# Kernel tuning notes

Measured on AMD Instinct MI355X. Metric: run time of the kernel, lower is better.

## Reference

```python
import jax, jax.numpy as jnp
import numpy as np

N_RAYS = 131072
N_SAMPLES = 64
N_IMPORTANCE = 128
NEAR, FAR = 2.0, 6.0


def setup_inputs() -> dict:
    key = jax.random.key(0)
    k1, k2, k3, k4 = jax.random.split(key, 4)
    rays_o = jax.random.normal(k1, (N_RAYS, 3), dtype=jnp.float32)
    rays_d = jax.random.normal(k2, (N_RAYS, 3), dtype=jnp.float32)
    # z_vals must be increasing along the sample axis (coarse sample output)
    z_vals = NEAR + (FAR - NEAR) * jnp.sort(
        jax.random.uniform(k3, (N_RAYS, N_SAMPLES), dtype=jnp.float32), axis=-1)
    weights = jax.random.uniform(k4, (N_RAYS, N_SAMPLES), dtype=jnp.float32)
    return {"rays_o": rays_o, "rays_d": rays_d, "z_vals": z_vals, "weights": weights}


def fine_sample(rays_o, rays_d, z_vals, weights):
    # z_vals: [N, S], weights: [N, S]; det=True (perturb == 0.0)
    z_mid = 0.5 * (z_vals[..., 1:] + z_vals[..., :-1])          # [N, S-1]
    w = weights[..., 1:-1] + 1e-5                               # [N, S-2]
    pdf = w / jnp.sum(w, axis=-1, keepdims=True)
    cdf = jnp.cumsum(pdf, axis=-1)
    cdf = jnp.concatenate([jnp.zeros_like(cdf[..., :1]), cdf], axis=-1)  # [N, S-1]

    u = jnp.linspace(0.0, 1.0, N_IMPORTANCE, dtype=cdf.dtype)
    u = jnp.broadcast_to(u, (cdf.shape[0], N_IMPORTANCE))       # [N, Ni]

    # per-ray binary search (right side), matching torch.searchsorted(right=True)
    inds = jax.vmap(lambda c, uu: jnp.searchsorted(c, uu, side='right'))(cdf, u)
    below = jnp.maximum(inds - 1, 0)
    above = jnp.minimum(inds, cdf.shape[-1] - 1)

    cdf_b = jnp.take_along_axis(cdf, below, axis=-1)
    cdf_a = jnp.take_along_axis(cdf, above, axis=-1)
    bins_b = jnp.take_along_axis(z_mid, below, axis=-1)
    bins_a = jnp.take_along_axis(z_mid, above, axis=-1)

    denom = cdf_a - cdf_b
    denom = jnp.where(denom < 1e-5, jnp.ones_like(denom), denom)
    t = (u - cdf_b) / denom
    z_samples = bins_b + t * (bins_a - bins_b)                  # [N, Ni]

    z_all = jnp.sort(jnp.concatenate([z_vals, z_samples], axis=-1), axis=-1)  # [N, S+Ni]
    pts = rays_o[:, None, :] + rays_d[:, None, :] * z_all[..., None]          # [N, S+Ni, 3]
    return pts, z_all


def reference(rays_o, rays_d, z_vals, weights):
    return fine_sample(rays_o, rays_d, z_vals, weights)
```

## Files before the change

### kernel.cpp

```cpp
#include <hip/hip_runtime.h>
#include <hip/hip_bf16.h>

#define S   64
#define NI  128
#define NT  192
#define WPB 4

__global__ __launch_bounds__(256) void nerf_fine_sample(
    const float* __restrict__ rays_o,
    const float* __restrict__ rays_d,
    const float* __restrict__ z_vals,
    const float* __restrict__ weights,
    float* __restrict__ out_pts,
    float* __restrict__ out_z)
{
    const int lane = threadIdx.x & 63;
    const int w    = threadIdx.x >> 6;
    const int ray  = blockIdx.x * WPB + w;

    __shared__ float s_zvals[WPB][S];
    __shared__ float s_zmid [WPB][S];
    __shared__ float s_cdf  [WPB][S];
    __shared__ float s_zs   [WPB][NI];
    __shared__ float s_zall [WPB][NT];
    __shared__ float s_od   [WPB][8];

    const float zv = z_vals[(size_t)ray * S + lane];
    const float wt = weights[(size_t)ray * S + lane];
    s_zvals[w][lane] = zv;
    if (lane < 6) {
        s_od[w][lane] = (lane < 3) ? rays_o[(size_t)ray * 3 + lane]
                                   : rays_d[(size_t)ray * 3 + (lane - 3)];
    }

    float zvn = __shfl_down(zv, 1);
    if (lane < S - 1) s_zmid[w][lane] = 0.5f * (zv + zvn);

    float x = (lane >= 1 && lane <= S - 2) ? (wt + 1e-5f) : 0.0f;
    float v = x;
    #pragma unroll
    for (int off = 1; off < 64; off <<= 1) {
        float n = __shfl_up(v, off);
        if (lane >= off) v += n;
    }
    const float total = __shfl(v, 63);
    const float inv   = 1.0f / total;
    if (lane <= S - 2) s_cdf[w][lane] = v * inv;

    __syncthreads();

    {
        const float* cdf  = s_cdf[w];
        const float* zmid = s_zmid[w];
        const float step = 1.0f / 127.0f;
        #pragma unroll
        for (int r = 0; r < 2; ++r) {
            const int k = lane + r * 64;
            float u = (k == NI - 1) ? 1.0f : (float)k * step;
            int lo = 0, hi = S - 1;
            while (lo < hi) {
                int m = (lo + hi) >> 1;
                if (cdf[m] <= u) lo = m + 1; else hi = m;
            }
            const int below = (lo > 0) ? lo - 1 : 0;
            const int above = (lo < S - 2) ? lo : S - 2;
            const float cb = cdf[below], ca = cdf[above];
            const float bb = zmid[below], ba = zmid[above];
            float denom = ca - cb;
            if (denom < 1e-5f) denom = 1.0f;
            const float t = (u - cb) / denom;
            s_zs[w][k] = bb + t * (ba - bb);
        }
    }
    __syncthreads();

    {
        const float* zs = s_zs[w];
        int lo = 0, hi = NI;
        while (lo < hi) {
            int m = (lo + hi) >> 1;
            if (zs[m] < zv) lo = m + 1; else hi = m;
        }
        s_zall[w][lane + lo] = zv;
    }
    {
        const float* za = s_zvals[w];
        #pragma unroll
        for (int r = 0; r < 2; ++r) {
            const int j = lane + r * 64;
            const float z = s_zs[w][j];
            int lo = 0, hi = S;
            while (lo < hi) {
                int m = (lo + hi) >> 1;
                if (za[m] <= z) lo = m + 1; else hi = m;
            }
            s_zall[w][j + lo] = z;
        }
    }
    __syncthreads();

    const float ox = s_od[w][0], oy = s_od[w][1], oz = s_od[w][2];
    const float dx = s_od[w][3], dy = s_od[w][4], dz = s_od[w][5];

    if (lane < NT / 4) {
        float4 q = ((const float4*)s_zall[w])[lane];
        ((float4*)(out_z + (size_t)ray * NT))[lane] = q;
    }

    float* po = out_pts + (size_t)ray * NT * 3;
    #pragma unroll
    for (int r = 0; r < 3; ++r) {
        const int e4 = lane + r * 64;
        if (e4 < 144) {
            float4 q;
            float qv[4];
            #pragma unroll
            for (int c = 0; c < 4; ++c) {
                const int e = e4 * 4 + c;
                const int s = e / 3;
                const int comp = e - 3 * s;
                const float z = s_zall[w][s];
                const float o = (comp == 0) ? ox : ((comp == 1) ? oy : oz);
                const float d = (comp == 0) ? dx : ((comp == 1) ? dy : dz);
                qv[c] = o + d * z;
            }
            q.x = qv[0]; q.y = qv[1]; q.z = qv[2]; q.w = qv[3];
            ((float4*)po)[e4] = q;
        }
    }
}

extern "C" void kernel_launch(void* const* d_in, const int* in_sizes, int n_in,
                              void* d_out, int out_size, void* d_ws, size_t ws_size,
                              hipStream_t stream) {
    const float* rays_o  = (const float*)d_in[0];
    const float* rays_d  = (const float*)d_in[1];
    const float* z_vals  = (const float*)d_in[2];
    const float* weights = (const float*)d_in[3];

    const int n_rays = in_sizes[0] / 3;
    float* out_pts = (float*)d_out;
    float* out_z   = out_pts + (size_t)n_rays * NT * 3;

    const int grid = n_rays / WPB;
    nerf_fine_sample<<<grid, 256, 0, stream>>>(rays_o, rays_d, z_vals, weights,
                                               out_pts, out_z);
}
```

Before: 478.2 us.

## Replace shared-memory staging and block barriers with wave shuffles

Keeps the CDF, midpoints and fine samples in registers and does every binary search through cross-lane shuffles with fixed iteration counts. This removes most LDS traffic and all three block-wide __syncthreads, leaving a single wave-level LDS wait before the merged output is read back. The point-writing loop is also simplified: each lane computes its o/d component rotation once and loads only two z values per float4. The risk is that shuffles cost about as much as LDS reads, and relying on a wave-local fence instead of a block barrier assumes each ray stays inside one wavefront.

```diff
diff --git a/kernel.cpp b/kernel.cpp
--- a/kernel.cpp
+++ b/kernel.cpp
@@ -1,10 +1,14 @@
 #include <hip/hip_runtime.h>
-#include <hip/hip_bf16.h>
 
-#define S   64
-#define NI  128
-#define NT  192
-#define WPB 4
+#define S    64
+#define NI   128
+#define NT   192
+#define WPB  4
+
+__device__ __forceinline__ void wave_lds_fence() {
+    asm volatile("s_waitcnt lgkmcnt(0)" ::: "memory");
+    __builtin_amdgcn_sched_barrier(0);
+}
 
 __global__ __launch_bounds__(256) void nerf_fine_sample(
     const float* __restrict__ rays_o,
@@ -18,115 +22,116 @@
     const int w    = threadIdx.x >> 6;
     const int ray  = blockIdx.x * WPB + w;
 
-    __shared__ float s_zvals[WPB][S];
-    __shared__ float s_zmid [WPB][S];
-    __shared__ float s_cdf  [WPB][S];
-    __shared__ float s_zs   [WPB][NI];
-    __shared__ float s_zall [WPB][NT];
-    __shared__ float s_od   [WPB][8];
+    __shared__ float s_zall[WPB][NT];
+    float* const zall = s_zall[w];
 
     const float zv = z_vals[(size_t)ray * S + lane];
     const float wt = weights[(size_t)ray * S + lane];
-    s_zvals[w][lane] = zv;
-    if (lane < 6) {
-        s_od[w][lane] = (lane < 3) ? rays_o[(size_t)ray * 3 + lane]
-                                   : rays_d[(size_t)ray * 3 + (lane - 3)];
+
+    const float ox = rays_o[(size_t)ray * 3 + 0];
+    const float oy = rays_o[(size_t)ray * 3 + 1];
+    const float oz = rays_o[(size_t)ray * 3 + 2];
+    const float dx = rays_d[(size_t)ray * 3 + 0];
+    const float dy = rays_d[(size_t)ray * 3 + 1];
+    const float dz = rays_d[(size_t)ray * 3 + 2];
+
+    const float zmid = 0.5f * (zv + __shfl_down(zv, 1));
+
+    float v = (lane >= 1 && lane <= S - 2) ? (wt + 1e-5f) : 0.0f;
+    #pragma unroll
+    for (int off = 1; off < 64; off <<= 1) {
+        const float n = __shfl_up(v, off);
+        if (lane >= off) v += n;
+    }
+    const float inv = 1.0f / __shfl(v, 63);
+    const float cdf = v * inv;
+
+    float zs0 = 0.0f, zs1 = 0.0f;
+    const float step = 1.0f / 127.0f;
+    #pragma unroll
+    for (int r = 0; r < 2; ++r) {
+        const int k = lane + (r << 6);
+        const float u = (k == NI - 1) ? 1.0f : (float)k * step;
+        int lo = 0, hi = S - 1;
+        #pragma unroll
+        for (int it = 0; it < 6; ++it) {
+            const int m = (lo + hi) >> 1;
+            const float c = __shfl(cdf, m);
+            if (c <= u) lo = m + 1; else hi = m;
+        }
+        const int below = (lo > 0) ? lo - 1 : 0;
+        const int above = (lo < S - 2) ? lo : S - 2;
+        const float cb = __shfl(cdf,  below);
+        const float ca = __shfl(cdf,  above);
+        const float bb = __shfl(zmid, below);
+        const float ba = __shfl(zmid, above);
+        float denom = ca - cb;
+        if (denom < 1e-5f) denom = 1.0f;
+        const float t = (u - cb) / denom;
+        const float z = bb + t * (ba - bb);
+        if (r == 0) zs0 = z; else zs1 = z;
     }
 
-    float zvn = __shfl_down(zv, 1);
-    if (lane < S - 1) s_zmid[w][lane] = 0.5f * (zv + zvn);
+    {
+        int lo = 0, hi = NI;
+        #pragma unroll
+        for (int it = 0; it < 8; ++it) {
+            const int m = (lo + hi) >> 1;
+            const float a  = __shfl(zs0, m & 63);
+            const float b  = __shfl(zs1, m & 63);
+            const float val = (m >= 64) ? b : a;
+            if (lo < hi) { if (val < zv) lo = m + 1; else hi = m; }
+        }
+        zall[lane + lo] = zv;
+    }
+    #pragma unroll
+    for (int r = 0; r < 2; ++r) {
+        const float z = (r == 0) ? zs0 : zs1;
+        int lo = 0, hi = S;
+        #pragma unroll
+        for (int it = 0; it < 7; ++it) {
+            const int m = (lo + hi) >> 1;
+            const float a = __shfl(zv, m & 63);
+            if (lo < hi) { if (a <= z) lo = m + 1; else hi = m; }
+        }
+        zall[lane + (r << 6) + lo] = z;
+    }
 
-    float x = (lane >= 1 && lane <= S - 2) ? (wt + 1e-5f) : 0.0f;
-    float v = x;
-    #pragma unroll
-    for (int off = 1; off < 64; off <<= 1) {
-        float n = __shfl_up(v, off);
-        if (lane >= off) v += n;
-    }
-    const float total = __shfl(v, 63);
-    const float inv   = 1.0f / total;
-    if (lane <= S - 2) s_cdf[w][lane] = v * inv;
-
-    __syncthreads();
-
-    {
-        const float* cdf  = s_cdf[w];
-        const float* zmid = s_zmid[w];
-        const float step = 1.0f / 127.0f;
-        #pragma unroll
-        for (int r = 0; r < 2; ++r) {
-            const int k = lane + r * 64;
-            float u = (k == NI - 1) ? 1.0f : (float)k * step;
-            int lo = 0, hi = S - 1;
-            while (lo < hi) {
-                int m = (lo + hi) >> 1;
-                if (cdf[m] <= u) lo = m + 1; else hi = m;
-            }
-            const int below = (lo > 0) ? lo - 1 : 0;
-            const int above = (lo < S - 2) ? lo : S - 2;
-            const float cb = cdf[below], ca = cdf[above];
-            const float bb = zmid[below], ba = zmid[above];
-            float denom = ca - cb;
-            if (denom < 1e-5f) denom = 1.0f;
-            const float t = (u - cb) / denom;
-            s_zs[w][k] = bb + t * (ba - bb);
-        }
-    }
-    __syncthreads();
-
-    {
-        const float* zs = s_zs[w];
-        int lo = 0, hi = NI;
-        while (lo < hi) {
-            int m = (lo + hi) >> 1;
-            if (zs[m] < zv) lo = m + 1; else hi = m;
-        }
-        s_zall[w][lane + lo] = zv;
-    }
-    {
-        const float* za = s_zvals[w];
-        #pragma unroll
-        for (int r = 0; r < 2; ++r) {
-            const int j = lane + r * 64;
-            const float z = s_zs[w][j];
-            int lo = 0, hi = S;
-            while (lo < hi) {
-                int m = (lo + hi) >> 1;
-                if (za[m] <= z) lo = m + 1; else hi = m;
-            }
-            s_zall[w][j + lo] = z;
-        }
-    }
-    __syncthreads();
-
-    const float ox = s_od[w][0], oy = s_od[w][1], oz = s_od[w][2];
-    const float dx = s_od[w][3], dy = s_od[w][4], dz = s_od[w][5];
+    wave_lds_fence();
 
     if (lane < NT / 4) {
-        float4 q = ((const float4*)s_zall[w])[lane];
+        const float4 q = ((const float4*)zall)[lane];
         ((float4*)(out_z + (size_t)ray * NT))[lane] = q;
     }
 
-    float* po = out_pts + (size_t)ray * NT * 3;
+    const int rem0 = lane - (lane / 3) * 3;
+    float o0 = (rem0 == 0) ? ox : ((rem0 == 1) ? oy : oz);
+    float o1 = (rem0 == 0) ? oy : ((rem0 == 1) ? oz : ox);
+    float o2 = (rem0 == 0) ? oz : ((rem0 == 1) ? ox : oy);
+    float d0 = (rem0 == 0) ? dx : ((rem0 == 1) ? dy : dz);
+    float d1 = (rem0 == 0) ? dy : ((rem0 == 1) ? dz : dx);
+    float d2 = (rem0 == 0) ? dz : ((rem0 == 1) ? dx : dy);
+    int rem = rem0;
+
+    float* const po = out_pts + (size_t)ray * (NT * 3);
     #pragma unroll
     for (int r = 0; r < 3; ++r) {
-        const int e4 = lane + r * 64;
+        const int e4 = lane + (r << 6);
         if (e4 < 144) {
+            const int b = e4 << 2;
+            const int s = b / 3;
+            const float z0 = zall[s];
+            const float z1 = zall[s + 1];
             float4 q;
-            float qv[4];
-            #pragma unroll
-            for (int c = 0; c < 4; ++c) {
-                const int e = e4 * 4 + c;
-                const int s = e / 3;
-                const int comp = e - 3 * s;
-                const float z = s_zall[w][s];
-                const float o = (comp == 0) ? ox : ((comp == 1) ? oy : oz);
-                const float d = (comp == 0) ? dx : ((comp == 1) ? dy : dz);
-                qv[c] = o + d * z;
-            }
-            q.x = qv[0]; q.y = qv[1]; q.z = qv[2]; q.w = qv[3];
+            q.x = fmaf(d0, z0, o0);
+            q.y = fmaf(d1, (rem == 2) ? z1 : z0, o1);
+            q.z = fmaf(d2, (rem == 0) ? z0 : z1, o2);
+            q.w = fmaf(d0, z1, o0);
             ((float4*)po)[e4] = q;
         }
+        const float to = o0; o0 = o1; o1 = o2; o2 = to;
+        const float td = d0; d0 = d1; d1 = d2; d2 = td;
+        rem = (rem == 2) ? 0 : rem + 1;
     }
 }
 
```

After: 463.6 us. 1.03x faster.
